# Optimization experiments

Measured on AMD Instinct MI355X. Metric: run time of the kernel, lower is better.

Reference implementation:

```python
import jax, jax.numpy as jnp
import numpy as np

B = 256          # graph pairs
MAX = 64         # max_node_set_size
D = 128          # node_state_dim
E_DIM = 64       # edge embedding dim
NODE_F = 32
EDGE_F = 16
AVG_DEG = 8
PROP_STEPS = 3
TEMP = 0.1


def _sizes():
    qs = 32 + (np.arange(B) % 33)   # query graph sizes in [32,64]
    cs = 33 + (np.arange(B) % 32)   # corpus graph sizes in [33,64]
    return qs, cs


def setup_inputs() -> dict:
    key = jax.random.key(0)
    ks = jax.random.split(key, 12)
    qs, cs = _sizes()
    sizes = np.empty(2 * B, dtype=np.int64)
    sizes[0::2] = qs
    sizes[1::2] = cs
    offsets = np.concatenate([[0], np.cumsum(sizes)])
    N = int(offsets[-1])
    rng = np.random.RandomState(0)
    frm, to, pos = [], [], []
    for g in range(2 * B):
        o, s = int(offsets[g]), int(sizes[g])
        ne = AVG_DEG * s
        frm.append(rng.randint(0, s, ne) + o)
        to.append(rng.randint(0, s, ne) + o)
        b, isq = g // 2, (g % 2 == 0)
        base = (0 if isq else B * MAX) + b * MAX
        pos.append(base + np.arange(s))
    from_idx = jnp.asarray(np.concatenate(frm), dtype=jnp.int32)
    to_idx = jnp.asarray(np.concatenate(to), dtype=jnp.int32)
    node_to_pos = jnp.asarray(np.concatenate(pos), dtype=jnp.int32)
    Etot = int(from_idx.shape[0])

    def w(k, shape):
        return jax.random.normal(k, shape, jnp.float32) * (1.0 / np.sqrt(shape[0]))

    return {
        "node_features": jax.random.normal(ks[0], (N, NODE_F), jnp.float32),
        "edge_features": jax.random.normal(ks[1], (Etot, EDGE_F), jnp.float32),
        "from_idx": from_idx,
        "to_idx": to_idx,
        "node_to_pos": node_to_pos,
        "query_sizes": jnp.asarray(qs, jnp.int32),
        "corpus_sizes": jnp.asarray(cs, jnp.int32),
        "W_node": w(ks[2], (NODE_F, D)), "b_node": jnp.zeros((D,), jnp.float32),
        "W_edge": w(ks[3], (EDGE_F, E_DIM)), "b_edge": jnp.zeros((E_DIM,), jnp.float32),
        "W_msg1": w(ks[4], (2 * D + E_DIM, 2 * D)), "b_msg1": jnp.zeros((2 * D,), jnp.float32),
        "W_msg2": w(ks[5], (2 * D, 2 * D)), "b_msg2": jnp.zeros((2 * D,), jnp.float32),
        "W_upd": w(ks[6], (3 * D, D)), "b_upd": jnp.zeros((D,), jnp.float32),
        "Wa1": w(ks[7], (D, D)), "ba1": jnp.zeros((D,), jnp.float32),
        "Wa2": w(ks[8], (D, D)), "ba2": jnp.zeros((D,), jnp.float32),
    }


def reference(node_features, edge_features, from_idx, to_idx, node_to_pos,
              query_sizes, corpus_sizes, W_node, b_node, W_edge, b_edge,
              W_msg1, b_msg1, W_msg2, b_msg2, W_upd, b_upd, Wa1, ba1, Wa2, ba2):
    N = node_features.shape[0]
    # GraphEncoder: single-layer node / edge MLPs
    h = node_features @ W_node + b_node
    e = edge_features @ W_edge + b_edge
    # GraphPropLayer applied propagation_steps times (residual node update)
    for _ in range(PROP_STEPS):
        edge_in = jnp.concatenate([h[from_idx], h[to_idx], e], axis=-1)  # [E, 2D+E_DIM]
        msg = jax.nn.relu(edge_in @ W_msg1 + b_msg1) @ W_msg2 + b_msg2   # [E, 2D]
        agg = jax.ops.segment_sum(msg, to_idx, num_segments=N)           # [N, 2D]
        h = h + (jnp.concatenate([h, agg], axis=-1) @ W_upd + b_upd)
    # split_and_stack: scatter flat node states into padded [B, MAX, D] query/corpus stacks
    flat = jnp.zeros((2 * B * MAX, D), h.dtype).at[node_to_pos].set(h)
    stacked = flat.reshape(2, B, MAX, D)
    sq, sc = stacked[0], stacked[1]

    def att_feat(x):
        return jax.nn.relu(x @ Wa1 + ba1) @ Wa2 + ba2

    mq = (jnp.arange(MAX)[None, :] < query_sizes[:, None]).astype(h.dtype)   # [B,MAX]
    mc = (jnp.arange(MAX)[None, :] < corpus_sizes[:, None]).astype(h.dtype)
    tq = att_feat(sq) * mq[:, :, None]   # graph_size_to_mask_map masking
    tc = att_feat(sc) * mc[:, :, None]
    logits = jnp.einsum('bqd,bcd->bqc', tq, tc) / TEMP
    pair_mask = mq[:, :, None] * mc[:, None, :]
    logits = jnp.where(pair_mask > 0, logits, -1e9)
    q_to_c = jax.nn.softmax(logits, axis=-1) * mq[:, :, None]   # row-stochastic over corpus
    c_to_q = jax.nn.softmax(logits, axis=-2) * mc[:, None, :]   # column-stochastic over query
    # feature_alignment_score / reversed_feature_alignment_score (hinge alignment)
    q_score = -jax.nn.relu(sq - jnp.einsum('bqc,bcd->bqd', q_to_c, sc)).sum((1, 2))
    c_score = -jax.nn.relu(sc - jnp.einsum('bqc,bqd->bcd', c_to_q, sq)).sum((1, 2))
    return jnp.minimum(q_score, c_score)   # attention_mode = 'min'
```

## Files before the change

kernel.cpp:

```cpp
#include <hip/hip_runtime.h>

#define D 128
#define EDIM 64
#define NODE_F 32
#define EDGE_F 16
#define B_PAIRS 256
#define MAXN 64
#define PROP_STEPS 3

typedef __attribute__((ext_vector_type(4))) short short4v;
typedef __attribute__((ext_vector_type(8))) short short8;
typedef __attribute__((ext_vector_type(16))) float floatx16;

__device__ __forceinline__ short f2bf(float x) {
  unsigned u = __float_as_uint(x);
  u = (u + 0x7fff + ((u >> 16) & 1)) >> 16;
  return (short)u;
}

__device__ __forceinline__ float bf2f(short s) {
  return __uint_as_float(((unsigned)(unsigned short)s) << 16);
}

__global__ __launch_bounds__(256) void init_kernel(
    const float* __restrict__ W_node, const float* __restrict__ W_edge,
    const float* __restrict__ W1, const float* __restrict__ W2,
    const float* __restrict__ Wu,
    const float* __restrict__ Wa1, const float* __restrict__ Wa2,
    short* __restrict__ Wfn, short* __restrict__ Wfe,
    short* __restrict__ Wf1a, short* __restrict__ Wf1b, short* __restrict__ Wf1e,
    short* __restrict__ Wf2, short* __restrict__ Wfu,
    short* __restrict__ Wfa1, short* __restrict__ Wfa2,
    const int* __restrict__ to_idx, int* __restrict__ deg,
    int* __restrict__ inv, int E)
{
  int bid = blockIdx.x;
  int t = threadIdx.x;
  if (bid >= 916) {
    int b2 = bid - 916;
    for (int e = b2 * 256 + t; e < E; e += 256 * 256)
      atomicAdd(&deg[to_idx[e]], 1);
    for (int i = b2 * 256 + t; i < 2 * B_PAIRS * MAXN; i += 256 * 256)
      inv[i] = -1;
    return;
  }
  int idx = bid * 256 + t;
  if (idx < 4096) {
    int step = idx >> 11, hi = (idx >> 10) & 1;
    int n = (idx >> 3) & 127, j = idx & 7;
    int k = step * 16 + hi * 8 + j;
    Wfn[idx] = f2bf(W_node[(size_t)k * 128 + n]);
  } else if (idx < 5120) {
    int i = idx - 4096;
    int hi = (i >> 9) & 1, n = (i >> 3) & 63, j = i & 7;
    int k = hi * 8 + j;
    Wfe[i] = f2bf(W_edge[(size_t)k * 64 + n]);
  } else if (idx < 37888) {
    int i = idx - 5120;
    int step = i >> 12, hi = (i >> 11) & 1;
    int n = (i >> 3) & 255, j = i & 7;
    int k = step * 16 + hi * 8 + j;
    Wf1a[i] = f2bf(W1[(size_t)k * 256 + n]);
  } else if (idx < 70656) {
    int i = idx - 37888;
    int step = i >> 12, hi = (i >> 11) & 1;
    int n = (i >> 3) & 255, j = i & 7;
    int k = step * 16 + hi * 8 + j;
    Wf1b[i] = f2bf(W1[(size_t)(128 + k) * 256 + n]);
  } else if (idx < 87040) {
    int i = idx - 70656;
    int step = i >> 12, hi = (i >> 11) & 1;
    int n = (i >> 3) & 255, j = i & 7;
    int k = step * 16 + hi * 8 + j;
    Wf1e[i] = f2bf(W1[(size_t)(256 + k) * 256 + n]);
  } else if (idx < 152576) {
    int i = idx - 87040;
    int step = i >> 12, hi = (i >> 11) & 1;
    int n = (i >> 3) & 255, j = i & 7;
    int k = step * 16 + hi * 8 + j;
    Wf2[i] = f2bf(W2[(size_t)k * 256 + n]);
  } else if (idx < 201728) {
    int i = idx - 152576;
    int step = i >> 11, hi = (i >> 10) & 1;
    int n = (i >> 3) & 127, j = i & 7;
    int k = step * 16 + hi * 8 + j;
    Wfu[i] = f2bf(Wu[(size_t)k * 128 + n]);
  } else if (idx < 218112) {
    int i = idx - 201728;
    int step = i >> 11, hi = (i >> 10) & 1;
    int n = (i >> 3) & 127, j = i & 7;
    int k = step * 16 + hi * 8 + j;
    Wfa1[i] = f2bf(Wa1[(size_t)k * 128 + n]);
  } else if (idx < 234496) {
    int i = idx - 218112;
    int step = i >> 11, hi = (i >> 10) & 1;
    int n = (i >> 3) & 127, j = i & 7;
    int k = step * 16 + hi * 8 + j;
    Wfa2[i] = f2bf(Wa2[(size_t)k * 128 + n]);
  }
}

__global__ __launch_bounds__(1024) void scan1(const int* __restrict__ deg,
                                              int* __restrict__ partials, int N)
{
  __shared__ int red[16];
  int t = threadIdx.x;
  int n = blockIdx.x * 1024 + t;
  int v = (n < N) ? deg[n] : 0;
  for (int off = 32; off > 0; off >>= 1) v += __shfl_down(v, off);
  if ((t & 63) == 0) red[t >> 6] = v;
  __syncthreads();
  if (t == 0) {
    int s = 0;
    #pragma unroll
    for (int i = 0; i < 16; i++) s += red[i];
    partials[blockIdx.x] = s;
  }
}

__global__ __launch_bounds__(64) void scan2(int* __restrict__ partials,
                                            int* __restrict__ offsets, int B, int N)
{
  __shared__ int sp[64];
  int t = threadIdx.x;
  sp[t] = (t < B) ? partials[t] : 0;
  __syncthreads();
  if (t == 0) {
    int run = 0;
    for (int i = 0; i < B; i++) { int v = sp[i]; sp[i] = run; run += v; }
    offsets[N] = run;
  }
  __syncthreads();
  if (t < B) partials[t] = sp[t];
}

__global__ __launch_bounds__(1024) void scan3(const int* __restrict__ deg,
                                              const int* __restrict__ partials,
                                              int* __restrict__ offsets,
                                              int* __restrict__ cursor,
                                              int* __restrict__ zflag,
                                              const int* __restrict__ pos,
                                              int* __restrict__ inv, int N)
{
  __shared__ int s[1024];
  int t = threadIdx.x;
  int n = blockIdx.x * 1024 + t;
  int d = (n < N) ? deg[n] : 0;
  s[t] = d;
  __syncthreads();
  for (int off = 1; off < 1024; off <<= 1) {
    int v = 0;
    if (t >= off) v = s[t - off];
    __syncthreads();
    if (t >= off) s[t] += v;
    __syncthreads();
  }
  if (n < N) {
    int off = partials[blockIdx.x] + s[t] - d;
    offsets[n] = off; cursor[n] = off;
    zflag[n] = (d == 0) || ((off >> 5) != ((off + d - 1) >> 5)) ? 1 : 0;
    inv[pos[n]] = n;
  }
}

__global__ __launch_bounds__(256) void scatter_csr(const int* __restrict__ to_idx,
                                                   int* __restrict__ cursor,
                                                   int* __restrict__ elist, int E)
{
  for (int e = blockIdx.x * 256 + threadIdx.x; e < E; e += gridDim.x * 256) {
    int pos = atomicAdd(&cursor[to_idx[e]], 1);
    elist[pos] = e;
  }
}

__global__ __launch_bounds__(256, 3) void enc_nodes_p(
    const float* __restrict__ nf, const short* __restrict__ Wfn,
    const float* __restrict__ b_node, float* __restrict__ h,
    short* __restrict__ hb,
    const short* __restrict__ Wf1a, const short* __restrict__ Wf1b,
    short* __restrict__ P1f, short* __restrict__ P2f, int N)
{
  __shared__ short sN[32 * 40];
  __shared__ short sH[32 * 136];
  int t = threadIdx.x;
  int ln = t & 63, w = t >> 6;
  int l31 = ln & 31, hi = ln >> 5;
  int n0 = blockIdx.x * 32;

  {
    int r = t >> 3, q = t & 7;
    float4 v = {0.f, 0.f, 0.f, 0.f};
    if (n0 + r < N) v = *(const float4*)(nf + (size_t)(n0 + r) * 32 + q * 4);
    short4v s;
    s[0] = f2bf(v.x); s[1] = f2bf(v.y); s[2] = f2bf(v.z); s[3] = f2bf(v.w);
    *(short4v*)(sN + r * 40 + q * 4) = s;
  }
  __syncthreads();

  int col = w * 32 + l31;
  {
    floatx16 acc;
    #pragma unroll
    for (int i = 0; i < 16; i++) acc[i] = 0.f;
    #pragma unroll
    for (int step = 0; step < 2; step++) {
      short8 a = *(const short8*)(sN + l31 * 40 + step * 16 + hi * 8);
      short8 b = *(const short8*)(Wfn + (size_t)(step * 2 + hi) * 1024 + col * 8);
      acc = __builtin_amdgcn_mfma_f32_32x32x16_bf16(a, b, acc, 0, 0, 0);
    }
    float bv = b_node[col];
    #pragma unroll
    for (int reg = 0; reg < 16; reg++) {
      int row = (reg & 3) + 8 * (reg >> 2) + 4 * hi;
      int n = n0 + row;
      float v = acc[reg] + bv;
      short bf = f2bf(v);
      if (n < N) {
        h[(size_t)n * 128 + col] = v;
        hb[(size_t)n * 128 + col] = bf;
      }
      sH[row * 136 + col] = bf;
    }
  }
  __syncthreads();

  int cb = w * 64;
  const int arow = l31 * 136;
  const int bc0 = (cb + l31) * 8, bc1 = (cb + 32 + l31) * 8;
  floatx16 acc[2][2];
  #pragma unroll
  for (int o = 0; o < 2; o++)
    #pragma unroll
    for (int ct = 0; ct < 2; ct++)
      #pragma unroll
      for (int i = 0; i < 16; i++) acc[o][ct][i] = 0.f;

  #pragma unroll
  for (int step = 0; step < 8; step++) {
    short8 a = *(const short8*)(sH + arow + step * 16 + hi * 8);
    short8 ba0 = *(const short8*)(Wf1a + (size_t)(step * 2 + hi) * 2048 + bc0);
    short8 ba1 = *(const short8*)(Wf1a + (size_t)(step * 2 + hi) * 2048 + bc1);
    short8 bb0 = *(const short8*)(Wf1b + (size_t)(step * 2 + hi) * 2048 + bc0);
    short8 bb1 = *(const short8*)(Wf1b + (size_t)(step * 2 + hi) * 2048 + bc1);
    acc[0][0] = __builtin_amdgcn_mfma_f32_32x32x16_bf16(a, ba0, acc[0][0], 0, 0, 0);
    acc[0][1] = __builtin_amdgcn_mfma_f32_32x32x16_bf16(a, ba1, acc[0][1], 0, 0, 0);
    acc[1][0] = __builtin_amdgcn_mfma_f32_32x32x16_bf16(a, bb0, acc[1][0], 0, 0, 0);
    acc[1][1] = __builtin_amdgcn_mfma_f32_32x32x16_bf16(a, bb1, acc[1][1], 0, 0, 0);
  }

  #pragma unroll
  for (int ct = 0; ct < 2; ct++) {
    int pcol = cb + ct * 32 + l31;
    #pragma unroll
    for (int reg = 0; reg < 16; reg++) {
      int row = (reg & 3) + 8 * (reg >> 2) + 4 * hi;
      int n = n0 + row;
      if (n < N) {
        P1f[(size_t)n * 256 + pcol] = f2bf(acc[0][ct][reg]);
        P2f[(size_t)n * 256 + pcol] = f2bf(acc[1][ct][reg]);
      }
    }
  }
}

__global__ __launch_bounds__(256, 6) void msg_agg(
    const float* __restrict__ ef, const int* __restrict__ elist,
    const short* __restrict__ Wfe, const float* __restrict__ b_edge,
    const short* __restrict__ Wf1e, const float* __restrict__ b1,
    const short* __restrict__ P1f, const short* __restrict__ P2f,
    const int* __restrict__ from_idx, const int* __restrict__ to_idx,
    const int* __restrict__ offsets,
    float* __restrict__ agg, int E)
{
  __shared__ short sE[32 * 24];
  __shared__ short sF[32 * 76];
  __shared__ short sA[32 * 264];
  __shared__ int eid_s[32];
  __shared__ int from_s[32], to_s[32];
  __shared__ int rend_s[32], inter_s[32];

  int t = threadIdx.x;
  int ln = t & 63, w = t >> 6;
  int l31 = ln & 31, hi = ln >> 5;
  int e0 = blockIdx.x * 32;

  if (t < 32) {
    int idx = e0 + t;
    int eid = (idx < E) ? elist[idx] : 0;
    eid_s[t] = eid;
    from_s[t] = from_idx[eid];
    to_s[t] = (idx < E) ? to_idx[eid] : -1;
  }
  __syncthreads();

  if (t < 32) {
    int nd = to_s[t];
    bool head = (t == 0) || (nd != to_s[t - 1]);
    if (head && nd >= 0) {
      int re = t + 1;
      while (re < 32 && to_s[re] == nd) re++;
      rend_s[t] = re;
      inter_s[t] = (offsets[nd] == e0 + t) && (offsets[nd + 1] == e0 + re) ? 1 : 0;
    }
  }

  if (t < 128) {
    int r = t >> 2, q = t & 3;
    float4 v = *(const float4*)(ef + (size_t)eid_s[r] * 16 + q * 4);
    short4v s;
    s[0] = f2bf(v.x); s[1] = f2bf(v.y); s[2] = f2bf(v.z); s[3] = f2bf(v.w);
    *(short4v*)(sE + r * 24 + q * 4) = s;
  }
  __syncthreads();

  if (w < 2) {
    int cbq = w * 32;
    floatx16 acc;
    #pragma unroll
    for (int i = 0; i < 16; i++) acc[i] = 0.f;
    short8 a = *(const short8*)(sE + l31 * 24 + hi * 8);
    short8 b = *(const short8*)(Wfe + (size_t)hi * 512 + (cbq + l31) * 8);
    acc = __builtin_amdgcn_mfma_f32_32x32x16_bf16(a, b, acc, 0, 0, 0);
    int col = cbq + l31;
    float bv = b_edge[col];
    #pragma unroll
    for (int reg = 0; reg < 16; reg++) {
      int row = (reg & 3) + 8 * (reg >> 2) + 4 * hi;
      sF[row * 76 + col] = f2bf(acc[reg] + bv);
    }
  }
  __syncthreads();

  {
    const int cb = w * 64;
    const int bc0 = (cb + l31) * 8, bc1 = (cb + 32 + l31) * 8;
    floatx16 acc[2];
    #pragma unroll
    for (int ct = 0; ct < 2; ct++)
      #pragma unroll
      for (int i = 0; i < 16; i++) acc[ct][i] = 0.f;

    #pragma unroll
    for (int step = 0; step < 4; step++) {
      short8 a = *(const short8*)(sF + l31 * 76 + step * 16 + hi * 8);
      short8 b0 = *(const short8*)(Wf1e + (size_t)(step * 2 + hi) * 2048 + bc0);
      short8 b1v = *(const short8*)(Wf1e + (size_t)(step * 2 + hi) * 2048 + bc1);
      acc[0] = __builtin_amdgcn_mfma_f32_32x32x16_bf16(a, b0,  acc[0], 0, 0, 0);
      acc[1] = __builtin_amdgcn_mfma_f32_32x32x16_bf16(a, b1v, acc[1], 0, 0, 0);
    }

    #pragma unroll
    for (int ct = 0; ct < 2; ct++) {
      int col = cb + ct * 32 + l31;
      float bv = b1[col];
      #pragma unroll
      for (int reg = 0; reg < 16; reg++) {
        int row = (reg & 3) + 8 * (reg >> 2) + 4 * hi;
        sA[row * 264 + col] = f2bf(acc[ct][reg] + bv);
      }
    }
  }
  __syncthreads();

  for (int i = t; i < 1024; i += 256) {
    int r = i >> 5, c8 = (i & 31) * 8;
    int nd = to_s[r]; if (nd < 0) nd = 0;
    short8 a = *(const short8*)(P1f + (size_t)from_s[r] * 256 + c8);
    short8 b = *(const short8*)(P2f + (size_t)nd * 256 + c8);
    short8 c = *(short8*)(sA + r * 264 + c8);
    short8 o;
    #pragma unroll
    for (int j = 0; j < 8; j++)
      o[j] = f2bf(fmaxf(bf2f(a[j]) + bf2f(b[j]) + bf2f(c[j]), 0.f));
    *(short8*)(sA + r * 264 + c8) = o;
  }
  __syncthreads();

  {
    int c = t;
    for (int r = 0; r < 32; ) {
      int nd = to_s[r];
      if (nd < 0) break;
      int re = rend_s[r];
      float a = 0.f;
      for (int i = r; i < re; i++)
        a += bf2f(sA[i * 264 + c]);
      float* dst = agg + (size_t)nd * 256 + c;
      if (inter_s[r]) *dst = a;
      else unsafeAtomicAdd(dst, a);
      r = re;
    }
  }
}

__global__ __launch_bounds__(256, 4) void update_mfma_p(
    float* __restrict__ h, short* __restrict__ hbf, float* __restrict__ agg,
    const short* __restrict__ Wf2, const float* __restrict__ b2,
    const int* __restrict__ deg,
    const short* __restrict__ Wfu, const float* __restrict__ bu,
    const short* __restrict__ Wf1a, const short* __restrict__ Wf1b,
    short* __restrict__ P1f, short* __restrict__ P2f,
    const int* __restrict__ zflag, int want_p, int N)
{
  __shared__ short sA2[32 * 136];
  __shared__ short sS[32 * 264];
  __shared__ int zf_s[32];
  __shared__ int deg_s[32];

  int t = threadIdx.x;
  int ln = t & 63, w = t >> 6;
  int l31 = ln & 31, hi = ln >> 5;
  int n0 = blockIdx.x * 32;

  if (t < 32) {
    zf_s[t] = (n0 + t < N) ? zflag[n0 + t] : 0;
    deg_s[t] = (n0 + t < N) ? deg[n0 + t] : 0;
  }

  for (int i = t; i < 512; i += 256) {
    int r = i >> 4, c = i & 15;
    short8 v = {0, 0, 0, 0, 0, 0, 0, 0};
    if (n0 + r < N) v = *(const short8*)(hbf + (size_t)(n0 + r) * 128 + c * 8);
    *(short8*)(sA2 + r * 136 + c * 8) = v;
  }
  for (int i = t; i < 2048; i += 256) {
    int r = i >> 6, c4 = i & 63;
    int2 pk = {0, 0};
    if (n0 + r < N) {
      float4 v = *(const float4*)(agg + (size_t)(n0 + r) * 256 + c4 * 4);
      pk.x = (int)(unsigned short)f2bf(v.x) | ((int)(unsigned short)f2bf(v.y) << 16);
      pk.y = (int)(unsigned short)f2bf(v.z) | ((int)(unsigned short)f2bf(v.w) << 16);
    }
    *(int2*)(sS + r * 264 + c4 * 4) = pk;
  }
  __syncthreads();

  {
    float4 z = {0.f, 0.f, 0.f, 0.f};
    for (int i = t; i < 2048; i += 256) {
      int r = i >> 6, c4 = i & 63;
      if (n0 + r < N && zf_s[r])
        *(float4*)(agg + (size_t)(n0 + r) * 256 + c4 * 4) = z;
    }
  }

  floatx16 macc[2];
  int cb2 = w * 64;
  {
    const int bc0 = (cb2 + l31) * 8, bc1 = (cb2 + 32 + l31) * 8;
    #pragma unroll
    for (int ct = 0; ct < 2; ct++)
      #pragma unroll
      for (int i = 0; i < 16; i++) macc[ct][i] = 0.f;

    #pragma unroll
    for (int step = 0; step < 16; step++) {
      short8 a = *(const short8*)(sS + l31 * 264 + step * 16 + hi * 8);
      short8 b0 = *(const short8*)(Wf2 + (size_t)(step * 2 + hi) * 2048 + bc0);
      short8 b1v = *(const short8*)(Wf2 + (size_t)(step * 2 + hi) * 2048 + bc1);
      macc[0] = __builtin_amdgcn_mfma_f32_32x32x16_bf16(a, b0,  macc[0], 0, 0, 0);
      macc[1] = __builtin_amdgcn_mfma_f32_32x32x16_bf16(a, b1v, macc[1], 0, 0, 0);
    }
  }
  __syncthreads();

  {
    #pragma unroll
    for (int ct = 0; ct < 2; ct++) {
      int col = cb2 + ct * 32 + l31;
      float bv2 = b2[col];
      #pragma unroll
      for (int reg = 0; reg < 16; reg++) {
        int row = (reg & 3) + 8 * (reg >> 2) + 4 * hi;
        sS[row * 264 + col] = f2bf(macc[ct][reg] + (float)deg_s[row] * bv2);
      }
    }
  }
  __syncthreads();

  const int bcol = (w * 32 + l31) * 8;

  floatx16 acc;
  #pragma unroll
  for (int i = 0; i < 16; i++) acc[i] = 0.f;

  {
    auto aptr = [&](int step) -> const short* {
      int kb = step * 16 + hi * 8;
      return (step < 8) ? (sA2 + l31 * 136 + kb) : (sS + l31 * 264 + (kb - 128));
    };
    short8 bbuf[3];
    #pragma unroll
    for (int s = 0; s < 3; s++)
      bbuf[s] = *(const short8*)(Wfu + (size_t)(s * 2 + hi) * 1024 + bcol);
    short8 abuf[2];
    abuf[0] = *(const short8*)aptr(0);
    #pragma unroll
    for (int step = 0; step < 24; step++) {
      if (step + 1 < 24)
        abuf[(step + 1) & 1] = *(const short8*)aptr(step + 1);
      acc = __builtin_amdgcn_mfma_f32_32x32x16_bf16(abuf[step & 1], bbuf[step % 3], acc, 0, 0, 0);
      if (step + 3 < 24)
        bbuf[step % 3] = *(const short8*)(Wfu + (size_t)((step + 3) * 2 + hi) * 1024 + bcol);
    }
  }

  __syncthreads();

  int col = w * 32 + l31;
  float bv = bu[col];
  #pragma unroll
  for (int reg = 0; reg < 16; reg++) {
    int row = (reg & 3) + 8 * (reg >> 2) + 4 * hi;
    int n = n0 + row;
    float nv = 0.f;
    if (n < N) nv = h[(size_t)n * 128 + col] + acc[reg] + bv;
    short bf = f2bf(nv);
    if (n < N) {
      h[(size_t)n * 128 + col] = nv;
      hbf[(size_t)n * 128 + col] = bf;
    }
    sA2[row * 136 + col] = bf;
  }

  if (!want_p) return;
  __syncthreads();

  int cb = w * 64;
  const int bc0 = (cb + l31) * 8, bc1 = (cb + 32 + l31) * 8;
  const int arow = l31 * 136;
  floatx16 pacc[2][2];
  #pragma unroll
  for (int o = 0; o < 2; o++)
    #pragma unroll
    for (int ct = 0; ct < 2; ct++)
      #pragma unroll
      for (int i = 0; i < 16; i++) pacc[o][ct][i] = 0.f;

  #pragma unroll
  for (int step = 0; step < 8; step++) {
    short8 a = *(const short8*)(sA2 + arow + step * 16 + hi * 8);
    short8 ba0 = *(const short8*)(Wf1a + (size_t)(step * 2 + hi) * 2048 + bc0);
    short8 ba1 = *(const short8*)(Wf1a + (size_t)(step * 2 + hi) * 2048 + bc1);
    short8 bb0 = *(const short8*)(Wf1b + (size_t)(step * 2 + hi) * 2048 + bc0);
    short8 bb1 = *(const short8*)(Wf1b + (size_t)(step * 2 + hi) * 2048 + bc1);
    pacc[0][0] = __builtin_amdgcn_mfma_f32_32x32x16_bf16(a, ba0, pacc[0][0], 0, 0, 0);
    pacc[0][1] = __builtin_amdgcn_mfma_f32_32x32x16_bf16(a, ba1, pacc[0][1], 0, 0, 0);
    pacc[1][0] = __builtin_amdgcn_mfma_f32_32x32x16_bf16(a, bb0, pacc[1][0], 0, 0, 0);
    pacc[1][1] = __builtin_amdgcn_mfma_f32_32x32x16_bf16(a, bb1, pacc[1][1], 0, 0, 0);
  }

  #pragma unroll
  for (int ct = 0; ct < 2; ct++) {
    int pcol = cb + ct * 32 + l31;
    #pragma unroll
    for (int reg = 0; reg < 16; reg++) {
      int row = (reg & 3) + 8 * (reg >> 2) + 4 * hi;
      int n = n0 + row;
      if (n < N) {
        P1f[(size_t)n * 256 + pcol] = f2bf(pacc[0][ct][reg]);
        P2f[(size_t)n * 256 + pcol] = f2bf(pacc[1][ct][reg]);
      }
    }
  }
}

__global__ __launch_bounds__(256, 3) void stack_attfeat(
    const float* __restrict__ h, const int* __restrict__ inv,
    const short* __restrict__ Wfa1, const float* __restrict__ ba1,
    const short* __restrict__ Wfa2, const float* __restrict__ ba2,
    const int* __restrict__ qsizes, const int* __restrict__ csizes,
    float* __restrict__ flat, short* __restrict__ flatT, short* __restrict__ tfb)
{
  __shared__ short sA[64 * 136];
  __shared__ int nd_s[64];

  int t = threadIdx.x;
  int ln = t & 63, w = t >> 6;
  int l31 = ln & 31, hi = ln >> 5;
  int r0 = blockIdx.x * 64;

  if (t < 64) nd_s[t] = inv[r0 + t];
  __syncthreads();

  for (int i = t; i < 1024; i += 256) {
    int r = i >> 4, c = (i & 15) * 8;
    int nd = nd_s[r];
    float4 v0 = {0.f, 0.f, 0.f, 0.f}, v1 = {0.f, 0.f, 0.f, 0.f};
    if (nd >= 0) {
      v0 = *(const float4*)(h + (size_t)nd * 128 + c);
      v1 = *(const float4*)(h + (size_t)nd * 128 + c + 4);
    }
    *(float4*)(flat + (size_t)(r0 + r) * 128 + c) = v0;
    *(float4*)(flat + (size_t)(r0 + r) * 128 + c + 4) = v1;
    short8 s;
    s[0] = f2bf(v0.x); s[1] = f2bf(v0.y); s[2] = f2bf(v0.z); s[3] = f2bf(v0.w);
    s[4] = f2bf(v1.x); s[5] = f2bf(v1.y); s[6] = f2bf(v1.z); s[7] = f2bf(v1.w);
    *(short8*)(sA + r * 136 + c) = s;
  }
  __syncthreads();

  for (int i = t; i < 8192; i += 256) {
    int d = i >> 6, r = i & 63;
    flatT[(size_t)blockIdx.x * 8192 + d * 64 + r] = sA[r * 136 + d];
  }

  const int arow0 = l31 * 136, arow1 = (32 + l31) * 136;
  const int bcol = (w * 32 + l31) * 8;
  int col = w * 32 + l31;

  floatx16 acc[2];
  #pragma unroll
  for (int rg = 0; rg < 2; rg++)
    #pragma unroll
    for (int i = 0; i < 16; i++) acc[rg][i] = 0.f;

  #pragma unroll
  for (int step = 0; step < 8; step++) {
    short8 a0 = *(const short8*)(sA + arow0 + step * 16 + hi * 8);
    short8 a1 = *(const short8*)(sA + arow1 + step * 16 + hi * 8);
    short8 bfr = *(const short8*)(Wfa1 + (size_t)(step * 2 + hi) * 1024 + bcol);
    acc[0] = __builtin_amdgcn_mfma_f32_32x32x16_bf16(a0, bfr, acc[0], 0, 0, 0);
    acc[1] = __builtin_amdgcn_mfma_f32_32x32x16_bf16(a1, bfr, acc[1], 0, 0, 0);
  }

  __syncthreads();
  {
    float bv = ba1[col];
    #pragma unroll
    for (int rg = 0; rg < 2; rg++)
      #pragma unroll
      for (int reg = 0; reg < 16; reg++) {
        int row = rg * 32 + (reg & 3) + 8 * (reg >> 2) + 4 * hi;
        sA[row * 136 + col] = f2bf(fmaxf(acc[rg][reg] + bv, 0.f));
      }
  }
  __syncthreads();

  floatx16 acc2[2];
  #pragma unroll
  for (int rg = 0; rg < 2; rg++)
    #pragma unroll
    for (int i = 0; i < 16; i++) acc2[rg][i] = 0.f;

  #pragma unroll
  for (int step = 0; step < 8; step++) {
    short8 a0 = *(const short8*)(sA + arow0 + step * 16 + hi * 8);
    short8 a1 = *(const short8*)(sA + arow1 + step * 16 + hi * 8);
    short8 bfr = *(const short8*)(Wfa2 + (size_t)(step * 2 + hi) * 1024 + bcol);
    acc2[0] = __builtin_amdgcn_mfma_f32_32x32x16_bf16(a0, bfr, acc2[0], 0, 0, 0);
    acc2[1] = __builtin_amdgcn_mfma_f32_32x32x16_bf16(a1, bfr, acc2[1], 0, 0, 0);
  }

  {
    float bv = ba2[col];
    #pragma unroll
    for (int rg = 0; rg < 2; rg++)
      #pragma unroll
      for (int reg = 0; reg < 16; reg++) {
        int row = r0 + rg * 32 + (reg & 3) + 8 * (reg >> 2) + 4 * hi;
        int part = row >> 14, b = (row >> 6) & 255, pp = row & 63;
        int sz = part ? csizes[b] : qsizes[b];
        float m = (pp < sz) ? 1.f : 0.f;
        tfb[(size_t)row * 128 + col] = f2bf((acc2[rg][reg] + bv) * m);
      }
  }
}

__global__ __launch_bounds__(256, 3) void score_kernel(
    const short* __restrict__ tfb, const float* __restrict__ flat,
    const short* __restrict__ flatT,
    const int* __restrict__ qsizes, const int* __restrict__ csizes,
    float* __restrict__ out)
{
  __shared__ float SL[64 * 65];
  __shared__ float SP2[64 * 65];
  __shared__ float rstat[128];
  __shared__ float cstat[128];
  __shared__ float red[8];

  int b = blockIdx.x, t = threadIdx.x;
  int ln = t & 63, w = t >> 6;
  int l31 = ln & 31, hi = ln >> 5;
  const short* tqb = tfb + (size_t)b * 8192;
  const short* tcb = tfb + (size_t)(256 + b) * 8192;
  const float* sq = flat + (size_t)b * 8192;
  const float* sc = flat + (size_t)(256 + b) * 8192;
  const short* sqT = flatT + (size_t)b * 8192;
  const short* scT = flatT + (size_t)(256 + b) * 8192;
  int qs = qsizes[b], cs = csizes[b];

  {
    int rowb = (w & 1) * 32, cbq = (w >> 1) * 32;
    floatx16 acc;
    #pragma unroll
    for (int i = 0; i < 16; i++) acc[i] = 0.f;
    #pragma unroll
    for (int step = 0; step < 8; step++) {
      short8 a  = *(const short8*)(tqb + (size_t)(rowb + l31) * 128 + step * 16 + hi * 8);
      short8 bf = *(const short8*)(tcb + (size_t)(cbq + l31) * 128 + step * 16 + hi * 8);
      acc = __builtin_amdgcn_mfma_f32_32x32x16_bf16(a, bf, acc, 0, 0, 0);
    }
    int ccol = cbq + l31;
    #pragma unroll
    for (int reg = 0; reg < 16; reg++) {
      int qrow = rowb + (reg & 3) + 8 * (reg >> 2) + 4 * hi;
      SL[qrow * 65 + ccol] = (qrow < qs && ccol < cs) ? acc[reg] * 10.0f : -1e9f;
    }
  }
  __syncthreads();

  {
    int q = t >> 2, g = t & 3;
    const float* row = SL + q * 65 + g * 16;
    float m = -1e30f;
    #pragma unroll
    for (int i = 0; i < 16; i++) m = fmaxf(m, row[i]);
    m = fmaxf(m, __shfl_xor(m, 1));
    m = fmaxf(m, __shfl_xor(m, 2));
    float s = 0.f;
    #pragma unroll
    for (int i = 0; i < 16; i++) s += __expf(row[i] - m);
    s += __shfl_xor(s, 1);
    s += __shfl_xor(s, 2);
    if (g == 0) { rstat[q] = m; rstat[64 + q] = 1.0f / s; }
  }
  {
    int c = t >> 2, g = t & 3;
    const float* colp = SL + (g * 16) * 65 + c;
    float m = -1e30f;
    #pragma unroll
    for (int i = 0; i < 16; i++) m = fmaxf(m, colp[i * 65]);
    m = fmaxf(m, __shfl_xor(m, 1));
    m = fmaxf(m, __shfl_xor(m, 2));
    float s = 0.f;
    #pragma unroll
    for (int i = 0; i < 16; i++) s += __expf(colp[i * 65] - m);
    s += __shfl_xor(s, 1);
    s += __shfl_xor(s, 2);
    if (g == 0) { cstat[c] = m; cstat[64 + c] = 1.0f / s; }
  }
  __syncthreads();

  {
    int q = t >> 2, g = t & 3;
    float rm = rstat[q], ri = rstat[64 + q];
    bool qv = q < qs;
    #pragma unroll
    for (int i = 0; i < 16; i++) {
      int c = g * 16 + i;
      float v = SL[q * 65 + c];
      SL[q * 65 + c]  = qv ? __expf(v - rm) * ri : 0.f;
      SP2[q * 65 + c] = (c < cs) ? __expf(v - cstat[c]) * cstat[64 + c] : 0.f;
    }
  }
  __syncthreads();

  int dcol = w * 32 + l31;
  floatx16 accq[2], accc[2];
  #pragma unroll
  for (int rt = 0; rt < 2; rt++) {
    #pragma unroll
    for (int i = 0; i < 16; i++) { accq[rt][i] = 0.f; accc[rt][i] = 0.f; }
  }

  #pragma unroll
  for (int rt = 0; rt < 2; rt++) {
    #pragma unroll
    for (int step = 0; step < 4; step++) {
      int kb = step * 16 + hi * 8;
      int row = rt * 32 + l31;
      short8 a;
      #pragma unroll
      for (int j = 0; j < 8; j++) a[j] = f2bf(SL[row * 65 + kb + j]);
      short8 bf = *(const short8*)(scT + (size_t)dcol * 64 + kb);
      accq[rt] = __builtin_amdgcn_mfma_f32_32x32x16_bf16(a, bf, accq[rt], 0, 0, 0);
    }
  }
  #pragma unroll
  for (int rt = 0; rt < 2; rt++) {
    #pragma unroll
    for (int step = 0; step < 4; step++) {
      int kb = step * 16 + hi * 8;
      int crow = rt * 32 + l31;
      short8 a;
      #pragma unroll
      for (int j = 0; j < 8; j++) a[j] = f2bf(SP2[(kb + j) * 65 + crow]);
      short8 bf = *(const short8*)(sqT + (size_t)dcol * 64 + kb);
      accc[rt] = __builtin_amdgcn_mfma_f32_32x32x16_bf16(a, bf, accc[rt], 0, 0, 0);
    }
  }

  float qpart = 0.f, cpart = 0.f;
  #pragma unroll
  for (int rt = 0; rt < 2; rt++) {
    #pragma unroll
    for (int reg = 0; reg < 16; reg++) {
      int row = rt * 32 + (reg & 3) + 8 * (reg >> 2) + 4 * hi;
      qpart += fmaxf(sq[(size_t)row * 128 + dcol] - accq[rt][reg], 0.f);
      cpart += fmaxf(sc[(size_t)row * 128 + dcol] - accc[rt][reg], 0.f);
    }
  }

  for (int off = 32; off > 0; off >>= 1) {
    qpart += __shfl_down(qpart, off);
    cpart += __shfl_down(cpart, off);
  }
  if ((t & 63) == 0) { red[w] = qpart; red[w + 4] = cpart; }
  __syncthreads();
  if (t == 0) {
    float qsum = red[0] + red[1] + red[2] + red[3];
    float csum = red[4] + red[5] + red[6] + red[7];
    out[b] = fminf(-qsum, -csum);
  }
}

extern "C" void kernel_launch(void* const* d_in, const int* in_sizes, int n_in,
                              void* d_out, int out_size, void* d_ws, size_t ws_size,
                              hipStream_t stream)
{
  const float* nf  = (const float*)d_in[0];
  const float* ef  = (const float*)d_in[1];
  const int* from_idx = (const int*)d_in[2];
  const int* to_idx   = (const int*)d_in[3];
  const int* pos      = (const int*)d_in[4];
  const int* qsz      = (const int*)d_in[5];
  const int* csz      = (const int*)d_in[6];
  const float* W_node = (const float*)d_in[7];
  const float* b_node = (const float*)d_in[8];
  const float* W_edge = (const float*)d_in[9];
  const float* b_edge = (const float*)d_in[10];
  const float* W1 = (const float*)d_in[11];
  const float* b1 = (const float*)d_in[12];
  const float* W2 = (const float*)d_in[13];
  const float* b2 = (const float*)d_in[14];
  const float* Wu = (const float*)d_in[15];
  const float* bu = (const float*)d_in[16];
  const float* Wa1 = (const float*)d_in[17];
  const float* ba1 = (const float*)d_in[18];
  const float* Wa2 = (const float*)d_in[19];
  const float* ba2 = (const float*)d_in[20];
  float* out = (float*)d_out;

  int N = in_sizes[0] / NODE_F;
  int E = in_sizes[1] / EDGE_F;
  int Epad32 = (E + 31) & ~31;
  int PAD = 2 * B_PAIRS * MAXN;
  int NB = (N + 1023) / 1024;

  float* h    = (float*)d_ws;
  float* agg  = h + (size_t)N * D;
  short* hb   = (short*)(agg + (size_t)N * 256);
  short* P1f  = hb + (size_t)N * D;
  short* P2f  = P1f + (size_t)N * 256;
  short* Wfn  = P2f + (size_t)N * 256;
  short* Wfe  = Wfn + 4096;
  short* Wf1a = Wfe + 1024;
  short* Wf1b = Wf1a + 32768;
  short* Wf1e = Wf1b + 32768;
  short* Wf2  = Wf1e + 16384;
  short* Wfu  = Wf2 + 65536;
  short* Wfa1 = Wfu + 49152;
  short* Wfa2 = Wfa1 + 16384;
  int*   deg     = (int*)(Wfa2 + 16384);
  int*   offsets = deg + N;
  int*   cursor  = offsets + N + 1;
  int*   elist   = cursor + N;
  int*   inv     = elist + E;
  int*   zflag   = inv + PAD;
  int*   partials = zflag + N;
  uintptr_t pb = ((uintptr_t)(partials + 64) + 15) & ~(uintptr_t)15;
  float* flat  = (float*)pb;
  short* flatT = (short*)(flat + (size_t)PAD * D);
  short* tfb16 = flatT + (size_t)PAD * D;

  hipMemsetAsync(deg, 0, (size_t)N * sizeof(int), stream);
  init_kernel<<<916 + 256, 256, 0, stream>>>(
      W_node, W_edge, W1, W2, Wu, Wa1, Wa2,
      Wfn, Wfe, Wf1a, Wf1b, Wf1e, Wf2, Wfu, Wfa1, Wfa2,
      to_idx, deg, inv, E);
  scan1<<<NB, 1024, 0, stream>>>(deg, partials, N);
  scan2<<<1, 64, 0, stream>>>(partials, offsets, NB, N);
  scan3<<<NB, 1024, 0, stream>>>(deg, partials, offsets, cursor, zflag, pos, inv, N);
  scatter_csr<<<256, 256, 0, stream>>>(to_idx, cursor, elist, E);

  enc_nodes_p<<<(N + 31) / 32, 256, 0, stream>>>(nf, Wfn, b_node, h, hb,
                                                 Wf1a, Wf1b, P1f, P2f, N);

  hipMemsetAsync(agg, 0, (size_t)N * 256 * sizeof(float), stream);

  for (int s = 0; s < PROP_STEPS; s++) {
    msg_agg<<<Epad32 / 32, 256, 0, stream>>>(ef, elist, Wfe, b_edge, Wf1e, b1,
                                             P1f, P2f, from_idx, to_idx, offsets,
                                             agg, E);
    update_mfma_p<<<(N + 31) / 32, 256, 0, stream>>>(h, hb, agg, Wf2, b2, deg,
                                                     Wfu, bu, Wf1a, Wf1b, P1f, P2f, zflag,
                                                     (s + 1 < PROP_STEPS) ? 1 : 0, N);
  }

  stack_attfeat<<<PAD / 64, 256, 0, stream>>>(h, inv, Wfa1, ba1, Wfa2, ba2,
                                              qsz, csz, flat, flatT, tfb16);
  score_kernel<<<B_PAIRS, 256, 0, stream>>>(tfb16, flat, flatT, qsz, csz, out);
}
```

Baseline: 383.3 us.

## Compute message first-layer per edge instead of precomputed per-node projections

Stops precomputing the per-node projections P1/P2 (h@W1a, h@W1b) in the encoder and update kernels. The message kernel now gathers bf16 node states for the from and to nodes and runs the full first-layer GEMM per edge with MFMA. This removes the P1f/P2f writes and the 256-wide gathers, and shrinks the encoder and update kernels. In exchange it does roughly AVG_DEG times more matrix work per edge, and msg_agg's occupancy hint is lowered. The bf16 rounding also changes slightly, since the sum now accumulates in fp32 before one rounding.

```diff
diff --git a/kernel.cpp b/kernel.cpp
--- a/kernel.cpp
+++ b/kernel.cpp
@@ -173,15 +173,12 @@
   }
 }
 
-__global__ __launch_bounds__(256, 3) void enc_nodes_p(
+__global__ __launch_bounds__(256, 4) void enc_nodes(
     const float* __restrict__ nf, const short* __restrict__ Wfn,
     const float* __restrict__ b_node, float* __restrict__ h,
-    short* __restrict__ hb,
-    const short* __restrict__ Wf1a, const short* __restrict__ Wf1b,
-    short* __restrict__ P1f, short* __restrict__ P2f, int N)
+    short* __restrict__ hb, int N)
 {
   __shared__ short sN[32 * 40];
-  __shared__ short sH[32 * 136];
   int t = threadIdx.x;
   int ln = t & 63, w = t >> 6;
   int l31 = ln & 31, hi = ln >> 5;
@@ -198,86 +195,46 @@
   __syncthreads();
 
   int col = w * 32 + l31;
-  {
-    floatx16 acc;
-    #pragma unroll
-    for (int i = 0; i < 16; i++) acc[i] = 0.f;
-    #pragma unroll
-    for (int step = 0; step < 2; step++) {
-      short8 a = *(const short8*)(sN + l31 * 40 + step * 16 + hi * 8);
-      short8 b = *(const short8*)(Wfn + (size_t)(step * 2 + hi) * 1024 + col * 8);
-      acc = __builtin_amdgcn_mfma_f32_32x32x16_bf16(a, b, acc, 0, 0, 0);
-    }
-    float bv = b_node[col];
-    #pragma unroll
-    for (int reg = 0; reg < 16; reg++) {
-      int row = (reg & 3) + 8 * (reg >> 2) + 4 * hi;
-      int n = n0 + row;
+  floatx16 acc;
+  #pragma unroll
+  for (int i = 0; i < 16; i++) acc[i] = 0.f;
+  #pragma unroll
+  for (int step = 0; step < 2; step++) {
+    short8 a = *(const short8*)(sN + l31 * 40 + step * 16 + hi * 8);
+    short8 b = *(const short8*)(Wfn + (size_t)(step * 2 + hi) * 1024 + col * 8);
+    acc = __builtin_amdgcn_mfma_f32_32x32x16_bf16(a, b, acc, 0, 0, 0);
+  }
+  float bv = b_node[col];
+  #pragma unroll
+  for (int reg = 0; reg < 16; reg++) {
+    int row = (reg & 3) + 8 * (reg >> 2) + 4 * hi;
+    int n = n0 + row;
+    if (n < N) {
       float v = acc[reg] + bv;
-      short bf = f2bf(v);
-      if (n < N) {
-        h[(size_t)n * 128 + col] = v;
-        hb[(size_t)n * 128 + col] = bf;
-      }
-      sH[row * 136 + col] = bf;
-    }
-  }
-  __syncthreads();
-
-  int cb = w * 64;
-  const int arow = l31 * 136;
-  const int bc0 = (cb + l31) * 8, bc1 = (cb + 32 + l31) * 8;
-  floatx16 acc[2][2];
-  #pragma unroll
-  for (int o = 0; o < 2; o++)
-    #pragma unroll
-    for (int ct = 0; ct < 2; ct++)
-      #pragma unroll
-      for (int i = 0; i < 16; i++) acc[o][ct][i] = 0.f;
-
-  #pragma unroll
-  for (int step = 0; step < 8; step++) {
-    short8 a = *(const short8*)(sH + arow + step * 16 + hi * 8);
-    short8 ba0 = *(const short8*)(Wf1a + (size_t)(step * 2 + hi) * 2048 + bc0);
-    short8 ba1 = *(const short8*)(Wf1a + (size_t)(step * 2 + hi) * 2048 + bc1);
-    short8 bb0 = *(const short8*)(Wf1b + (size_t)(step * 2 + hi) * 2048 + bc0);
-    short8 bb1 = *(const short8*)(Wf1b + (size_t)(step * 2 + hi) * 2048 + bc1);
-    acc[0][0] = __builtin_amdgcn_mfma_f32_32x32x16_bf16(a, ba0, acc[0][0], 0, 0, 0);
-    acc[0][1] = __builtin_amdgcn_mfma_f32_32x32x16_bf16(a, ba1, acc[0][1], 0, 0, 0);
-    acc[1][0] = __builtin_amdgcn_mfma_f32_32x32x16_bf16(a, bb0, acc[1][0], 0, 0, 0);
-    acc[1][1] = __builtin_amdgcn_mfma_f32_32x32x16_bf16(a, bb1, acc[1][1], 0, 0, 0);
-  }
-
-  #pragma unroll
-  for (int ct = 0; ct < 2; ct++) {
-    int pcol = cb + ct * 32 + l31;
-    #pragma unroll
-    for (int reg = 0; reg < 16; reg++) {
-      int row = (reg & 3) + 8 * (reg >> 2) + 4 * hi;
-      int n = n0 + row;
-      if (n < N) {
-        P1f[(size_t)n * 256 + pcol] = f2bf(acc[0][ct][reg]);
-        P2f[(size_t)n * 256 + pcol] = f2bf(acc[1][ct][reg]);
-      }
-    }
-  }
-}
-
-__global__ __launch_bounds__(256, 6) void msg_agg(
+      h[(size_t)n * 128 + col] = v;
+      hb[(size_t)n * 128 + col] = f2bf(v);
+    }
+  }
+}
+
+__global__ __launch_bounds__(256, 5) void msg_agg(
     const float* __restrict__ ef, const int* __restrict__ elist,
     const short* __restrict__ Wfe, const float* __restrict__ b_edge,
     const short* __restrict__ Wf1e, const float* __restrict__ b1,
-    const short* __restrict__ P1f, const short* __restrict__ P2f,
+    const short* __restrict__ Wf1a, const short* __restrict__ Wf1b,
+    const short* __restrict__ hbf,
     const int* __restrict__ from_idx, const int* __restrict__ to_idx,
     const int* __restrict__ offsets,
     float* __restrict__ agg, int E)
 {
   __shared__ short sE[32 * 24];
   __shared__ short sF[32 * 76];
-  __shared__ short sA[32 * 264];
+  __shared__ short sH[2 * 32 * 136];
   __shared__ int eid_s[32];
   __shared__ int from_s[32], to_s[32];
   __shared__ int rend_s[32], inter_s[32];
+
+  short* sA = sH;
 
   int t = threadIdx.x;
   int ln = t & 63, w = t >> 6;
@@ -311,68 +268,76 @@
     s[0] = f2bf(v.x); s[1] = f2bf(v.y); s[2] = f2bf(v.z); s[3] = f2bf(v.w);
     *(short4v*)(sE + r * 24 + q * 4) = s;
   }
+  for (int i = t; i < 1024; i += 256) {
+    int which = i >> 9, r = (i >> 4) & 31, c = i & 15;
+    int nd = which ? to_s[r] : from_s[r];
+    if (nd < 0) nd = 0;
+    short8 v = *(const short8*)(hbf + (size_t)nd * 128 + c * 8);
+    *(short8*)(sH + which * 4352 + r * 136 + c * 8) = v;
+  }
   __syncthreads();
 
   if (w < 2) {
     int cbq = w * 32;
-    floatx16 acc;
-    #pragma unroll
-    for (int i = 0; i < 16; i++) acc[i] = 0.f;
+    floatx16 acc1;
+    #pragma unroll
+    for (int i = 0; i < 16; i++) acc1[i] = 0.f;
     short8 a = *(const short8*)(sE + l31 * 24 + hi * 8);
     short8 b = *(const short8*)(Wfe + (size_t)hi * 512 + (cbq + l31) * 8);
-    acc = __builtin_amdgcn_mfma_f32_32x32x16_bf16(a, b, acc, 0, 0, 0);
+    acc1 = __builtin_amdgcn_mfma_f32_32x32x16_bf16(a, b, acc1, 0, 0, 0);
     int col = cbq + l31;
     float bv = b_edge[col];
     #pragma unroll
     for (int reg = 0; reg < 16; reg++) {
       int row = (reg & 3) + 8 * (reg >> 2) + 4 * hi;
-      sF[row * 76 + col] = f2bf(acc[reg] + bv);
-    }
-  }
-  __syncthreads();
-
-  {
-    const int cb = w * 64;
-    const int bc0 = (cb + l31) * 8, bc1 = (cb + 32 + l31) * 8;
-    floatx16 acc[2];
-    #pragma unroll
-    for (int ct = 0; ct < 2; ct++)
-      #pragma unroll
-      for (int i = 0; i < 16; i++) acc[ct][i] = 0.f;
-
-    #pragma unroll
-    for (int step = 0; step < 4; step++) {
-      short8 a = *(const short8*)(sF + l31 * 76 + step * 16 + hi * 8);
-      short8 b0 = *(const short8*)(Wf1e + (size_t)(step * 2 + hi) * 2048 + bc0);
-      short8 b1v = *(const short8*)(Wf1e + (size_t)(step * 2 + hi) * 2048 + bc1);
-      acc[0] = __builtin_amdgcn_mfma_f32_32x32x16_bf16(a, b0,  acc[0], 0, 0, 0);
-      acc[1] = __builtin_amdgcn_mfma_f32_32x32x16_bf16(a, b1v, acc[1], 0, 0, 0);
-    }
-
-    #pragma unroll
-    for (int ct = 0; ct < 2; ct++) {
-      int col = cb + ct * 32 + l31;
-      float bv = b1[col];
-      #pragma unroll
-      for (int reg = 0; reg < 16; reg++) {
-        int row = (reg & 3) + 8 * (reg >> 2) + 4 * hi;
-        sA[row * 264 + col] = f2bf(acc[ct][reg] + bv);
-      }
-    }
-  }
-  __syncthreads();
-
-  for (int i = t; i < 1024; i += 256) {
-    int r = i >> 5, c8 = (i & 31) * 8;
-    int nd = to_s[r]; if (nd < 0) nd = 0;
-    short8 a = *(const short8*)(P1f + (size_t)from_s[r] * 256 + c8);
-    short8 b = *(const short8*)(P2f + (size_t)nd * 256 + c8);
-    short8 c = *(short8*)(sA + r * 264 + c8);
-    short8 o;
-    #pragma unroll
-    for (int j = 0; j < 8; j++)
-      o[j] = f2bf(fmaxf(bf2f(a[j]) + bf2f(b[j]) + bf2f(c[j]), 0.f));
-    *(short8*)(sA + r * 264 + c8) = o;
+      sF[row * 76 + col] = f2bf(acc1[reg] + bv);
+    }
+  }
+  __syncthreads();
+
+  const int cb = w * 64;
+  const int bc0 = (cb + l31) * 8, bc1 = (cb + 32 + l31) * 8;
+  floatx16 acc[2];
+  #pragma unroll
+  for (int ct = 0; ct < 2; ct++)
+    #pragma unroll
+    for (int i = 0; i < 16; i++) acc[ct][i] = 0.f;
+
+  #pragma unroll
+  for (int step = 0; step < 4; step++) {
+    short8 a = *(const short8*)(sF + l31 * 76 + step * 16 + hi * 8);
+    short8 b0 = *(const short8*)(Wf1e + (size_t)(step * 2 + hi) * 2048 + bc0);
+    short8 b1v = *(const short8*)(Wf1e + (size_t)(step * 2 + hi) * 2048 + bc1);
+    acc[0] = __builtin_amdgcn_mfma_f32_32x32x16_bf16(a, b0,  acc[0], 0, 0, 0);
+    acc[1] = __builtin_amdgcn_mfma_f32_32x32x16_bf16(a, b1v, acc[1], 0, 0, 0);
+  }
+  #pragma unroll
+  for (int step = 0; step < 8; step++) {
+    short8 a = *(const short8*)(sH + l31 * 136 + step * 16 + hi * 8);
+    short8 b0 = *(const short8*)(Wf1a + (size_t)(step * 2 + hi) * 2048 + bc0);
+    short8 b1v = *(const short8*)(Wf1a + (size_t)(step * 2 + hi) * 2048 + bc1);
+    acc[0] = __builtin_amdgcn_mfma_f32_32x32x16_bf16(a, b0,  acc[0], 0, 0, 0);
+    acc[1] = __builtin_amdgcn_mfma_f32_32x32x16_bf16(a, b1v, acc[1], 0, 0, 0);
+  }
+  #pragma unroll
+  for (int step = 0; step < 8; step++) {
+    short8 a = *(const short8*)(sH + 4352 + l31 * 136 + step * 16 + hi * 8);
+    short8 b0 = *(const short8*)(Wf1b + (size_t)(step * 2 + hi) * 2048 + bc0);
+    short8 b1v = *(const short8*)(Wf1b + (size_t)(step * 2 + hi) * 2048 + bc1);
+    acc[0] = __builtin_amdgcn_mfma_f32_32x32x16_bf16(a, b0,  acc[0], 0, 0, 0);
+    acc[1] = __builtin_amdgcn_mfma_f32_32x32x16_bf16(a, b1v, acc[1], 0, 0, 0);
+  }
+  __syncthreads();
+
+  #pragma unroll
+  for (int ct = 0; ct < 2; ct++) {
+    int col = cb + ct * 32 + l31;
+    float bv = b1[col];
+    #pragma unroll
+    for (int reg = 0; reg < 16; reg++) {
+      int row = (reg & 3) + 8 * (reg >> 2) + 4 * hi;
+      sA[row * 264 + col] = f2bf(fmaxf(acc[ct][reg] + bv, 0.f));
+    }
   }
   __syncthreads();
 
@@ -393,14 +358,12 @@
   }
 }
 
-__global__ __launch_bounds__(256, 4) void update_mfma_p(
+__global__ __launch_bounds__(256, 4) void update_mfma(
     float* __restrict__ h, short* __restrict__ hbf, float* __restrict__ agg,
     const short* __restrict__ Wf2, const float* __restrict__ b2,
     const int* __restrict__ deg,
     const short* __restrict__ Wfu, const float* __restrict__ bu,
-    const short* __restrict__ Wf1a, const short* __restrict__ Wf1b,
-    short* __restrict__ P1f, short* __restrict__ P2f,
-    const int* __restrict__ zflag, int want_p, int N)
+    const int* __restrict__ zflag, int N)
 {
   __shared__ short sA2[32 * 136];
   __shared__ short sS[32 * 264];
@@ -505,62 +468,16 @@
     }
   }
 
-  __syncthreads();
-
   int col = w * 32 + l31;
   float bv = bu[col];
   #pragma unroll
   for (int reg = 0; reg < 16; reg++) {
     int row = (reg & 3) + 8 * (reg >> 2) + 4 * hi;
     int n = n0 + row;
-    float nv = 0.f;
-    if (n < N) nv = h[(size_t)n * 128 + col] + acc[reg] + bv;
-    short bf = f2bf(nv);
     if (n < N) {
+      float nv = h[(size_t)n * 128 + col] + acc[reg] + bv;
       h[(size_t)n * 128 + col] = nv;
-      hbf[(size_t)n * 128 + col] = bf;
-    }
-    sA2[row * 136 + col] = bf;
-  }
-
-  if (!want_p) return;
-  __syncthreads();
-
-  int cb = w * 64;
-  const int bc0 = (cb + l31) * 8, bc1 = (cb + 32 + l31) * 8;
-  const int arow = l31 * 136;
-  floatx16 pacc[2][2];
-  #pragma unroll
-  for (int o = 0; o < 2; o++)
-    #pragma unroll
-    for (int ct = 0; ct < 2; ct++)
-      #pragma unroll
-      for (int i = 0; i < 16; i++) pacc[o][ct][i] = 0.f;
-
-  #pragma unroll
-  for (int step = 0; step < 8; step++) {
-    short8 a = *(const short8*)(sA2 + arow + step * 16 + hi * 8);
-    short8 ba0 = *(const short8*)(Wf1a + (size_t)(step * 2 + hi) * 2048 + bc0);
-    short8 ba1 = *(const short8*)(Wf1a + (size_t)(step * 2 + hi) * 2048 + bc1);
-    short8 bb0 = *(const short8*)(Wf1b + (size_t)(step * 2 + hi) * 2048 + bc0);
-    short8 bb1 = *(const short8*)(Wf1b + (size_t)(step * 2 + hi) * 2048 + bc1);
-    pacc[0][0] = __builtin_amdgcn_mfma_f32_32x32x16_bf16(a, ba0, pacc[0][0], 0, 0, 0);
-    pacc[0][1] = __builtin_amdgcn_mfma_f32_32x32x16_bf16(a, ba1, pacc[0][1], 0, 0, 0);
-    pacc[1][0] = __builtin_amdgcn_mfma_f32_32x32x16_bf16(a, bb0, pacc[1][0], 0, 0, 0);
-    pacc[1][1] = __builtin_amdgcn_mfma_f32_32x32x16_bf16(a, bb1, pacc[1][1], 0, 0, 0);
-  }
-
-  #pragma unroll
-  for (int ct = 0; ct < 2; ct++) {
-    int pcol = cb + ct * 32 + l31;
-    #pragma unroll
-    for (int reg = 0; reg < 16; reg++) {
-      int row = (reg & 3) + 8 * (reg >> 2) + 4 * hi;
-      int n = n0 + row;
-      if (n < N) {
-        P1f[(size_t)n * 256 + pcol] = f2bf(pacc[0][ct][reg]);
-        P2f[(size_t)n * 256 + pcol] = f2bf(pacc[1][ct][reg]);
-      }
+      hbf[(size_t)n * 128 + col] = f2bf(nv);
     }
   }
 }
@@ -884,18 +801,16 @@
   scan3<<<NB, 1024, 0, stream>>>(deg, partials, offsets, cursor, zflag, pos, inv, N);
   scatter_csr<<<256, 256, 0, stream>>>(to_idx, cursor, elist, E);
 
-  enc_nodes_p<<<(N + 31) / 32, 256, 0, stream>>>(nf, Wfn, b_node, h, hb,
-                                                 Wf1a, Wf1b, P1f, P2f, N);
+  enc_nodes<<<(N + 31) / 32, 256, 0, stream>>>(nf, Wfn, b_node, h, hb, N);
 
   hipMemsetAsync(agg, 0, (size_t)N * 256 * sizeof(float), stream);
 
   for (int s = 0; s < PROP_STEPS; s++) {
     msg_agg<<<Epad32 / 32, 256, 0, stream>>>(ef, elist, Wfe, b_edge, Wf1e, b1,
-                                             P1f, P2f, from_idx, to_idx, offsets,
-                                             agg, E);
-    update_mfma_p<<<(N + 31) / 32, 256, 0, stream>>>(h, hb, agg, Wf2, b2, deg,
-                                                     Wfu, bu, Wf1a, Wf1b, P1f, P2f, zflag,
-                                                     (s + 1 < PROP_STEPS) ? 1 : 0, N);
+                                             Wf1a, Wf1b, hb,
+                                             from_idx, to_idx, offsets, agg, E);
+    update_mfma<<<(N + 31) / 32, 256, 0, stream>>>(h, hb, agg, Wf2, b2, deg,
+                                                   Wfu, bu, zflag, N);
   }
 
   stack_attfeat<<<PAD / 64, 256, 0, stream>>>(h, inv, Wfa1, ba1, Wfa2, ba2,
```

Result: slower. 425.0 us (+10.9%).
